# Optimization experiments

Measured on AMD Instinct MI355X. Metric: run time of the kernel, lower is better.

The kernel has to match this reference:

```python
import jax, jax.numpy as jnp
import numpy as np

N_NODES = 100000


def setup_inputs() -> dict:
    key = jax.random.key(0)
    k1, k2, k3, k4 = jax.random.split(key, 4)
    N, E, D = N_NODES, 1200000, 64
    graph_embedding = jax.random.normal(k1, (N, D), dtype=jnp.float32)
    e_feat = jax.random.normal(k2, (E,), dtype=jnp.float32)
    src_idx = jax.random.randint(k3, (E,), 0, N, dtype=jnp.int32)
    dst_idx = jax.random.randint(k4, (E,), 0, N, dtype=jnp.int32)
    return {"graph_embedding": graph_embedding, "e_feat": e_feat,
            "src_idx": src_idx, "dst_idx": dst_idx}


def reference(graph_embedding, e_feat, src_idx, dst_idx):
    # message per edge: concat(src node feature [E,D], edge feature [E,1]) -> [E,D+1]
    e = e_feat.reshape(-1, 1).astype(jnp.float32)          # [E,1]
    msg = jnp.concatenate([graph_embedding[src_idx], e], axis=1)  # [E,D+1]
    # scatter-sum messages to destination nodes -> [N,D+1]
    res = jax.ops.segment_sum(msg, dst_idx, num_segments=N_NODES)
    return res
```

## Files before the change

kernel.cpp:

```cpp
#include <hip/hip_runtime.h>
#include <hip/hip_fp16.h>


#define NB_SHIFT 6
#define BNODES   64
#define SRC_BITS 17
#define SRC_MASK ((1 << SRC_BITS) - 1)
#define BIN_S    4096
#define BIN_T    512
#define MAXNB    2048

__global__ __launch_bounds__(BIN_T) void convhist_kernel(const float* __restrict__ g,
                                                         __half* __restrict__ h,
                                                         int n_emb, int c_blocks,
                                                         const int* __restrict__ dst,
                                                         int* __restrict__ counts,
                                                         int E, int NB) {
    __shared__ int cnt[MAXNB];
    int t = threadIdx.x;

    if (blockIdx.x < c_blocks) {
        int i = (blockIdx.x * BIN_T + t) * 8;
        if (i + 7 < n_emb) {
            float4 a = *(const float4*)(g + i);
            float4 b = *(const float4*)(g + i + 4);
            __half2 h0 = __floats2half2_rn(a.x, a.y);
            __half2 h1 = __floats2half2_rn(a.z, a.w);
            __half2 h2 = __floats2half2_rn(b.x, b.y);
            __half2 h3 = __floats2half2_rn(b.z, b.w);
            int4 o;
            o.x = *(int*)&h0; o.y = *(int*)&h1; o.z = *(int*)&h2; o.w = *(int*)&h3;
            *(int4*)(h + i) = o;
        } else {
            for (int k = i; k < n_emb; ++k) h[k] = __float2half(g[k]);
        }
        return;
    }

    int hb = blockIdx.x - c_blocks;
    for (int i = t; i < MAXNB; i += BIN_T) cnt[i] = 0;
    __syncthreads();
    int e0 = hb * BIN_S + t * 8;
    if (e0 + 7 < E) {
        int4 a = *(const int4*)(dst + e0);
        int4 b = *(const int4*)(dst + e0 + 4);
        atomicAdd(&cnt[a.x >> NB_SHIFT], 1);
        atomicAdd(&cnt[a.y >> NB_SHIFT], 1);
        atomicAdd(&cnt[a.z >> NB_SHIFT], 1);
        atomicAdd(&cnt[a.w >> NB_SHIFT], 1);
        atomicAdd(&cnt[b.x >> NB_SHIFT], 1);
        atomicAdd(&cnt[b.y >> NB_SHIFT], 1);
        atomicAdd(&cnt[b.z >> NB_SHIFT], 1);
        atomicAdd(&cnt[b.w >> NB_SHIFT], 1);
    } else {
        for (int k = e0; k < E; ++k) atomicAdd(&cnt[dst[k] >> NB_SHIFT], 1);
    }
    __syncthreads();
    for (int i = t; i < NB; i += BIN_T)
        if (cnt[i]) atomicAdd(&counts[i], cnt[i]);
}

__global__ void scan_kernel(const int* __restrict__ counts,
                            int* __restrict__ goff, int* __restrict__ gcur,
                            int NB) {
    __shared__ int sh[1024];
    int t = threadIdx.x;
    int c0 = (2 * t     < NB) ? counts[2 * t]     : 0;
    int c1 = (2 * t + 1 < NB) ? counts[2 * t + 1] : 0;
    int s  = c0 + c1;
    sh[t] = s;
    __syncthreads();
    for (int o = 1; o < 1024; o <<= 1) {
        int u = (t >= o) ? sh[t - o] : 0;
        __syncthreads();
        sh[t] += u;
        __syncthreads();
    }
    int ex = sh[t] - s;
    if (2 * t < NB)     { goff[2 * t]     = ex;      gcur[2 * t]     = ex;      }
    if (2 * t + 1 < NB) { goff[2 * t + 1] = ex + c0; gcur[2 * t + 1] = ex + c0; }
    if (t == 1023) goff[NB] = sh[1023];
}

__global__ __launch_bounds__(BIN_T) void bin_kernel(const int* __restrict__ src,
                                                    const float* __restrict__ ef,
                                                    const int* __restrict__ dst,
                                                    int* __restrict__ gcur,
                                                    int2* __restrict__ gpay, int E) {
    __shared__ int cnt[MAXNB];
    __shared__ int lbase[MAXNB];
    __shared__ int wsum[8];
    __shared__ int wbase[8];
    __shared__ int2 stage[BIN_S];
    __shared__ unsigned short sbuck[BIN_S];

    const int t    = threadIdx.x;
    const int lane = t & 63;
    const int wv   = t >> 6;

    for (int i = t; i < MAXNB; i += BIN_T) cnt[i] = 0;
    __syncthreads();

    int e0 = blockIdx.x * BIN_S + t * 8;
    int dv[8], sv[8], bk[8], rk[8];
    float ev[8];

    if (e0 + 7 < E) {
        *(int4*)&dv[0]   = *(const int4*)(dst + e0);
        *(int4*)&dv[4]   = *(const int4*)(dst + e0 + 4);
        *(int4*)&sv[0]   = *(const int4*)(src + e0);
        *(int4*)&sv[4]   = *(const int4*)(src + e0 + 4);
        *(float4*)&ev[0] = *(const float4*)(ef + e0);
        *(float4*)&ev[4] = *(const float4*)(ef + e0 + 4);
#pragma unroll
        for (int k = 0; k < 8; ++k) {
            bk[k] = dv[k] >> NB_SHIFT;
            rk[k] = atomicAdd(&cnt[bk[k]], 1);
        }
    } else {
#pragma unroll
        for (int k = 0; k < 8; ++k) {
            if (e0 + k < E) {
                dv[k] = dst[e0 + k];
                sv[k] = src[e0 + k];
                ev[k] = ef[e0 + k];
                bk[k] = dv[k] >> NB_SHIFT;
                rk[k] = atomicAdd(&cnt[bk[k]], 1);
            } else {
                bk[k] = -1;
            }
        }
    }
    __syncthreads();

    int c0 = cnt[4 * t], c1 = cnt[4 * t + 1], c2 = cnt[4 * t + 2], c3 = cnt[4 * t + 3];
    int ts = c0 + c1 + c2 + c3;
    int incl = ts;
#pragma unroll
    for (int o = 1; o < 64; o <<= 1) {
        int u = __shfl_up(incl, o);
        if (lane >= o) incl += u;
    }
    if (lane == 63) wsum[wv] = incl;
    __syncthreads();
    if (t < 8) {
        int v = wsum[t];
        int inc = v;
#pragma unroll
        for (int o = 1; o < 8; o <<= 1) {
            int u = __shfl_up(inc, o);
            if (t >= o) inc += u;
        }
        wbase[t] = inc - v;
    }
    __syncthreads();
    int ex = wbase[wv] + (incl - ts);
    lbase[4 * t]     = ex;
    lbase[4 * t + 1] = ex + c0;
    lbase[4 * t + 2] = ex + c0 + c1;
    lbase[4 * t + 3] = ex + c0 + c1 + c2;
    __syncthreads();

#pragma unroll
    for (int k = 0; k < 8; ++k) {
        if (bk[k] >= 0) {
            int pos = lbase[bk[k]] + rk[k];
            stage[pos] = make_int2(((dv[k] & (BNODES - 1)) << SRC_BITS) | sv[k],
                                   __float_as_int(ev[k]));
            sbuck[pos] = (unsigned short)bk[k];
        }
    }
    for (int i = t; i < MAXNB; i += BIN_T) {
        int c = cnt[i];
        cnt[i] = (c ? atomicAdd(&gcur[i], c) : 0) - lbase[i];
    }
    __syncthreads();

    int s_total = min(BIN_S, E - blockIdx.x * BIN_S);
    for (int i = t; i < s_total; i += BIN_T) {
        int b = sbuck[i];
        gpay[cnt[b] + i] = stage[i];
    }
}

__global__ __launch_bounds__(256) void bsort_kernel(const int2* __restrict__ gpay,
                                                    const int* __restrict__ goff,
                                                    int* __restrict__ gsrc2,
                                                    int* __restrict__ noff,
                                                    float* __restrict__ out,
                                                    int N, int E) {
    __shared__ int   cnt[BNODES];
    __shared__ int   cur[BNODES];
    __shared__ float esum[BNODES];

    const int t  = threadIdx.x;
    const int b  = blockIdx.x;
    const int lo = goff[b];
    const int hi = goff[b + 1];

    if (t < BNODES) { cnt[t] = 0; esum[t] = 0.f; }
    __syncthreads();

    for (int i = lo + t; i < hi; i += 256)
        atomicAdd(&cnt[gpay[i].x >> SRC_BITS], 1);
    __syncthreads();

    if (t < 64) {
        int v = cnt[t];
        int inc = v;
#pragma unroll
        for (int o = 1; o < 64; o <<= 1) {
            int u = __shfl_up(inc, o);
            if (t >= o) inc += u;
        }
        int base = lo + inc - v;
        cur[t] = base;
        int node = b * BNODES + t;
        if (node <= N) noff[node] = base;
    }
    if (b == 0 && t == 0) noff[N] = E;
    __syncthreads();

    for (int i = lo + t; i < hi; i += 256) {
        int2 p = gpay[i];
        int  r = p.x >> SRC_BITS;
        int pos = atomicAdd(&cur[r], 1);
        gsrc2[pos] = p.x & SRC_MASK;
        atomicAdd(&esum[r], __int_as_float(p.y));
    }
    __syncthreads();

    if (t < 64) {
        int node = b * BNODES + t;
        if (node < N) out[(size_t)node * 65 + 64] = esum[t];
    }
}

__global__ void gather_h_kernel(const __half* __restrict__ hg,
                                const int* __restrict__ gs,
                                const int* __restrict__ noff,
                                float* __restrict__ out, int N) {
    int wid  = (blockIdx.x * blockDim.x + threadIdx.x) >> 6;
    int lane = threadIdx.x & 63;
    if (wid >= N) return;

    int beg = noff[wid];
    int end = noff[wid + 1];

    float a0 = 0.f, a1 = 0.f, a2 = 0.f, a3 = 0.f;
    float a4 = 0.f, a5 = 0.f, a6 = 0.f, a7 = 0.f;
    int j = beg;
    for (; j + 7 < end; j += 8) {
        int s0 = gs[j];     int s1 = gs[j + 1];
        int s2 = gs[j + 2]; int s3 = gs[j + 3];
        int s4 = gs[j + 4]; int s5 = gs[j + 5];
        int s6 = gs[j + 6]; int s7 = gs[j + 7];
        a0 += __half2float(hg[(size_t)s0 * 64 + lane]);
        a1 += __half2float(hg[(size_t)s1 * 64 + lane]);
        a2 += __half2float(hg[(size_t)s2 * 64 + lane]);
        a3 += __half2float(hg[(size_t)s3 * 64 + lane]);
        a4 += __half2float(hg[(size_t)s4 * 64 + lane]);
        a5 += __half2float(hg[(size_t)s5 * 64 + lane]);
        a6 += __half2float(hg[(size_t)s6 * 64 + lane]);
        a7 += __half2float(hg[(size_t)s7 * 64 + lane]);
    }
    for (; j + 3 < end; j += 4) {
        int s0 = gs[j];     int s1 = gs[j + 1];
        int s2 = gs[j + 2]; int s3 = gs[j + 3];
        a0 += __half2float(hg[(size_t)s0 * 64 + lane]);
        a1 += __half2float(hg[(size_t)s1 * 64 + lane]);
        a2 += __half2float(hg[(size_t)s2 * 64 + lane]);
        a3 += __half2float(hg[(size_t)s3 * 64 + lane]);
    }
    for (; j < end; ++j) {
        a0 += __half2float(hg[(size_t)gs[j] * 64 + lane]);
    }
    out[(size_t)wid * 65 + lane] = ((a0 + a1) + (a2 + a3)) + ((a4 + a5) + (a6 + a7));
}


__global__ void atomic_fallback_kernel(const float* __restrict__ gemb,
                                       const float* __restrict__ efeat,
                                       const int* __restrict__ src,
                                       const int* __restrict__ dst,
                                       float* __restrict__ out, int E) {
    int eidx = blockIdx.x * 4 + (threadIdx.x >> 6);
    int lane = threadIdx.x & 63;
    if (eidx >= E) return;
    int s = src[eidx];
    int d = dst[eidx];
    float v = gemb[(size_t)s * 64 + lane];
    atomicAdd(&out[(size_t)d * 65 + lane], v);
    if (lane == 0) atomicAdd(&out[(size_t)d * 65 + 64], efeat[eidx]);
}


extern "C" void kernel_launch(void* const* d_in, const int* in_sizes, int n_in,
                              void* d_out, int out_size, void* d_ws, size_t ws_size,
                              hipStream_t stream) {
    const float* gemb  = (const float*)d_in[0];
    const float* efeat = (const float*)d_in[1];
    const int*   src   = (const int*)d_in[2];
    const int*   dst   = (const int*)d_in[3];
    float*       out   = (float*)d_out;

    const int N  = in_sizes[0] / 64;
    const int E  = in_sizes[1];
    const int NB = (N + BNODES - 1) >> NB_SHIFT;

    auto aln = [](size_t x) { return (x + 15) & ~(size_t)15; };
    size_t off_counts = 0;
    size_t off_goff   = off_counts + aln((size_t)NB * 4);
    size_t off_gcur   = off_goff   + aln((size_t)(NB + 1) * 4);
    size_t off_noff   = off_gcur   + aln((size_t)NB * 4);
    size_t off_gpay   = off_noff   + aln((size_t)(N + 1) * 4);
    size_t off_gsrc2  = off_gpay   + aln((size_t)E * 8);
    size_t off_hg     = off_gsrc2  + aln((size_t)E * 4);
    size_t needed     = off_hg     + (size_t)N * 64 * 2;

    if (N > (1 << SRC_BITS) || NB > MAXNB || ws_size < needed) {
        hipMemsetAsync(d_out, 0, (size_t)out_size * sizeof(float), stream);
        int blocks = (E + 3) / 4;
        atomic_fallback_kernel<<<blocks, 256, 0, stream>>>(gemb, efeat, src, dst, out, E);
        return;
    }

    char*   ws     = (char*)d_ws;
    int*    counts = (int*)(ws + off_counts);
    int*    goff   = (int*)(ws + off_goff);
    int*    gcur   = (int*)(ws + off_gcur);
    int*    noff   = (int*)(ws + off_noff);
    int2*   gpay   = (int2*)(ws + off_gpay);
    int*    gsrc2  = (int*)(ws + off_gsrc2);
    __half* hg     = (__half*)(ws + off_hg);

    hipMemsetAsync(counts, 0, (size_t)NB * 4, stream);

    int n_emb    = N * 64;
    int c_blocks = (n_emb + BIN_T * 8 - 1) / (BIN_T * 8);
    int h_blocks = (E + BIN_S - 1) / BIN_S;
    convhist_kernel<<<c_blocks + h_blocks, BIN_T, 0, stream>>>(
        gemb, hg, n_emb, c_blocks, dst, counts, E, NB);

    scan_kernel<<<1, 1024, 0, stream>>>(counts, goff, gcur, NB);
    bin_kernel<<<h_blocks, BIN_T, 0, stream>>>(src, efeat, dst, gcur, gpay, E);
    bsort_kernel<<<NB, 256, 0, stream>>>(gpay, goff, gsrc2, noff, out, N, E);

    int g_blocks = (N + 3) / 4;
    gather_h_kernel<<<g_blocks, 256, 0, stream>>>(hg, gsrc2, noff, out, N);
}
```

Baseline: 110.1 us.

## Fold bucket scan into bin kernel, split payload arrays, gather half2 per lane

```diff
diff --git a/kernel.cpp b/kernel.cpp
--- a/kernel.cpp
+++ b/kernel.cpp
@@ -60,43 +60,60 @@
         if (cnt[i]) atomicAdd(&counts[i], cnt[i]);
 }
 
-__global__ void scan_kernel(const int* __restrict__ counts,
-                            int* __restrict__ goff, int* __restrict__ gcur,
-                            int NB) {
-    __shared__ int sh[1024];
-    int t = threadIdx.x;
-    int c0 = (2 * t     < NB) ? counts[2 * t]     : 0;
-    int c1 = (2 * t + 1 < NB) ? counts[2 * t + 1] : 0;
-    int s  = c0 + c1;
-    sh[t] = s;
-    __syncthreads();
-    for (int o = 1; o < 1024; o <<= 1) {
-        int u = (t >= o) ? sh[t - o] : 0;
-        __syncthreads();
-        sh[t] += u;
-        __syncthreads();
-    }
-    int ex = sh[t] - s;
-    if (2 * t < NB)     { goff[2 * t]     = ex;      gcur[2 * t]     = ex;      }
-    if (2 * t + 1 < NB) { goff[2 * t + 1] = ex + c0; gcur[2 * t + 1] = ex + c0; }
-    if (t == 1023) goff[NB] = sh[1023];
-}
-
 __global__ __launch_bounds__(BIN_T) void bin_kernel(const int* __restrict__ src,
                                                     const float* __restrict__ ef,
                                                     const int* __restrict__ dst,
-                                                    int* __restrict__ gcur,
-                                                    int2* __restrict__ gpay, int E) {
+                                                    const int* __restrict__ counts,
+                                                    int* __restrict__ gcur0,
+                                                    int* __restrict__ goff,
+                                                    int* __restrict__ gkey,
+                                                    float* __restrict__ gef,
+                                                    int E, int NB) {
     __shared__ int cnt[MAXNB];
     __shared__ int lbase[MAXNB];
     __shared__ int wsum[8];
     __shared__ int wbase[8];
-    __shared__ int2 stage[BIN_S];
+    __shared__ int   skey[BIN_S];
+    __shared__ float sef[BIN_S];
     __shared__ unsigned short sbuck[BIN_S];
 
     const int t    = threadIdx.x;
     const int lane = t & 63;
     const int wv   = t >> 6;
+
+    int4 gc = *(const int4*)(counts + 4 * t);
+    int gts = gc.x + gc.y + gc.z + gc.w;
+    int ginc = gts;
+#pragma unroll
+    for (int o = 1; o < 64; o <<= 1) {
+        int u = __shfl_up(ginc, o);
+        if (lane >= o) ginc += u;
+    }
+    if (lane == 63) wsum[wv] = ginc;
+    __syncthreads();
+    if (t < 8) {
+        int v = wsum[t];
+        int inc = v;
+#pragma unroll
+        for (int o = 1; o < 8; o <<= 1) {
+            int u = __shfl_up(inc, o);
+            if (t >= o) inc += u;
+        }
+        wbase[t] = inc - v;
+    }
+    __syncthreads();
+    int gex = wbase[wv] + (ginc - gts);
+    int sb0 = gex;
+    int sb1 = sb0 + gc.x;
+    int sb2 = sb1 + gc.y;
+    int sb3 = sb2 + gc.z;
+    if (blockIdx.x == 0) {
+        if (4 * t     <= NB) goff[4 * t]     = sb0;
+        if (4 * t + 1 <= NB) goff[4 * t + 1] = sb1;
+        if (4 * t + 2 <= NB) goff[4 * t + 2] = sb2;
+        if (4 * t + 3 <= NB) goff[4 * t + 3] = sb3;
+    }
+    __syncthreads();
 
     for (int i = t; i < MAXNB; i += BIN_T) cnt[i] = 0;
     __syncthreads();
@@ -154,36 +171,46 @@
         wbase[t] = inc - v;
     }
     __syncthreads();
-    int ex = wbase[wv] + (incl - ts);
-    lbase[4 * t]     = ex;
-    lbase[4 * t + 1] = ex + c0;
-    lbase[4 * t + 2] = ex + c0 + c1;
-    lbase[4 * t + 3] = ex + c0 + c1 + c2;
+    int ex  = wbase[wv] + (incl - ts);
+    int lb0 = ex;
+    int lb1 = lb0 + c0;
+    int lb2 = lb1 + c1;
+    int lb3 = lb2 + c2;
+    lbase[4 * t]     = lb0;
+    lbase[4 * t + 1] = lb1;
+    lbase[4 * t + 2] = lb2;
+    lbase[4 * t + 3] = lb3;
     __syncthreads();
 
 #pragma unroll
     for (int k = 0; k < 8; ++k) {
         if (bk[k] >= 0) {
             int pos = lbase[bk[k]] + rk[k];
-            stage[pos] = make_int2(((dv[k] & (BNODES - 1)) << SRC_BITS) | sv[k],
-                                   __float_as_int(ev[k]));
+            skey[pos]  = ((dv[k] & (BNODES - 1)) << SRC_BITS) | sv[k];
+            sef[pos]   = ev[k];
             sbuck[pos] = (unsigned short)bk[k];
         }
     }
-    for (int i = t; i < MAXNB; i += BIN_T) {
-        int c = cnt[i];
-        cnt[i] = (c ? atomicAdd(&gcur[i], c) : 0) - lbase[i];
+    {
+        int f;
+        f = (c0 ? sb0 + atomicAdd(&gcur0[4 * t],     c0) : 0) - lb0; cnt[4 * t]     = f;
+        f = (c1 ? sb1 + atomicAdd(&gcur0[4 * t + 1], c1) : 0) - lb1; cnt[4 * t + 1] = f;
+        f = (c2 ? sb2 + atomicAdd(&gcur0[4 * t + 2], c2) : 0) - lb2; cnt[4 * t + 2] = f;
+        f = (c3 ? sb3 + atomicAdd(&gcur0[4 * t + 3], c3) : 0) - lb3; cnt[4 * t + 3] = f;
     }
     __syncthreads();
 
     int s_total = min(BIN_S, E - blockIdx.x * BIN_S);
     for (int i = t; i < s_total; i += BIN_T) {
         int b = sbuck[i];
-        gpay[cnt[b] + i] = stage[i];
-    }
-}
-
-__global__ __launch_bounds__(256) void bsort_kernel(const int2* __restrict__ gpay,
+        int p = cnt[b] + i;
+        gkey[p] = skey[i];
+        gef[p]  = sef[i];
+    }
+}
+
+__global__ __launch_bounds__(256) void bsort_kernel(const int* __restrict__ gkey,
+                                                    const float* __restrict__ gef,
                                                     const int* __restrict__ goff,
                                                     int* __restrict__ gsrc2,
                                                     int* __restrict__ noff,
@@ -202,7 +229,7 @@
     __syncthreads();
 
     for (int i = lo + t; i < hi; i += 256)
-        atomicAdd(&cnt[gpay[i].x >> SRC_BITS], 1);
+        atomicAdd(&cnt[gkey[i] >> SRC_BITS], 1);
     __syncthreads();
 
     if (t < 64) {
@@ -222,11 +249,11 @@
     __syncthreads();
 
     for (int i = lo + t; i < hi; i += 256) {
-        int2 p = gpay[i];
-        int  r = p.x >> SRC_BITS;
+        int k = gkey[i];
+        int r = k >> SRC_BITS;
         int pos = atomicAdd(&cur[r], 1);
-        gsrc2[pos] = p.x & SRC_MASK;
-        atomicAdd(&esum[r], __int_as_float(p.y));
+        gsrc2[pos] = k & SRC_MASK;
+        atomicAdd(&esum[r], gef[i]);
     }
     __syncthreads();
 
@@ -236,46 +263,66 @@
     }
 }
 
-__global__ void gather_h_kernel(const __half* __restrict__ hg,
-                                const int* __restrict__ gs,
-                                const int* __restrict__ noff,
-                                float* __restrict__ out, int N) {
+__global__ void gather_h2_kernel(const __half* __restrict__ hg,
+                                 const int* __restrict__ gs,
+                                 const int* __restrict__ noff,
+                                 float* __restrict__ out, int N) {
     int wid  = (blockIdx.x * blockDim.x + threadIdx.x) >> 6;
     int lane = threadIdx.x & 63;
     if (wid >= N) return;
 
+    const unsigned int* __restrict__ hg32 = (const unsigned int*)hg;
+    const int hl  = lane >> 5;
+    const int l32 = lane & 31;
+
     int beg = noff[wid];
     int end = noff[wid + 1];
 
-    float a0 = 0.f, a1 = 0.f, a2 = 0.f, a3 = 0.f;
-    float a4 = 0.f, a5 = 0.f, a6 = 0.f, a7 = 0.f;
+    float ax0 = 0.f, ay0 = 0.f, ax1 = 0.f, ay1 = 0.f;
+    float ax2 = 0.f, ay2 = 0.f, ax3 = 0.f, ay3 = 0.f;
+
     int j = beg;
-    for (; j + 7 < end; j += 8) {
-        int s0 = gs[j];     int s1 = gs[j + 1];
-        int s2 = gs[j + 2]; int s3 = gs[j + 3];
-        int s4 = gs[j + 4]; int s5 = gs[j + 5];
-        int s6 = gs[j + 6]; int s7 = gs[j + 7];
-        a0 += __half2float(hg[(size_t)s0 * 64 + lane]);
-        a1 += __half2float(hg[(size_t)s1 * 64 + lane]);
-        a2 += __half2float(hg[(size_t)s2 * 64 + lane]);
-        a3 += __half2float(hg[(size_t)s3 * 64 + lane]);
-        a4 += __half2float(hg[(size_t)s4 * 64 + lane]);
-        a5 += __half2float(hg[(size_t)s5 * 64 + lane]);
-        a6 += __half2float(hg[(size_t)s6 * 64 + lane]);
-        a7 += __half2float(hg[(size_t)s7 * 64 + lane]);
-    }
-    for (; j + 3 < end; j += 4) {
-        int s0 = gs[j];     int s1 = gs[j + 1];
-        int s2 = gs[j + 2]; int s3 = gs[j + 3];
-        a0 += __half2float(hg[(size_t)s0 * 64 + lane]);
-        a1 += __half2float(hg[(size_t)s1 * 64 + lane]);
-        a2 += __half2float(hg[(size_t)s2 * 64 + lane]);
-        a3 += __half2float(hg[(size_t)s3 * 64 + lane]);
-    }
-    for (; j < end; ++j) {
-        a0 += __half2float(hg[(size_t)gs[j] * 64 + lane]);
-    }
-    out[(size_t)wid * 65 + lane] = ((a0 + a1) + (a2 + a3)) + ((a4 + a5) + (a6 + a7));
+    for (; j + 15 < end; j += 16) {
+        int s0 = gs[j +  0 + hl]; int s1 = gs[j +  2 + hl];
+        int s2 = gs[j +  4 + hl]; int s3 = gs[j +  6 + hl];
+        int s4 = gs[j +  8 + hl]; int s5 = gs[j + 10 + hl];
+        int s6 = gs[j + 12 + hl]; int s7 = gs[j + 14 + hl];
+        unsigned int u0 = hg32[(size_t)s0 * 32 + l32];
+        unsigned int u1 = hg32[(size_t)s1 * 32 + l32];
+        unsigned int u2 = hg32[(size_t)s2 * 32 + l32];
+        unsigned int u3 = hg32[(size_t)s3 * 32 + l32];
+        unsigned int u4 = hg32[(size_t)s4 * 32 + l32];
+        unsigned int u5 = hg32[(size_t)s5 * 32 + l32];
+        unsigned int u6 = hg32[(size_t)s6 * 32 + l32];
+        unsigned int u7 = hg32[(size_t)s7 * 32 + l32];
+        __half2 h0 = *(__half2*)&u0; ax0 += __half2float(h0.x); ay0 += __half2float(h0.y);
+        __half2 h1 = *(__half2*)&u1; ax1 += __half2float(h1.x); ay1 += __half2float(h1.y);
+        __half2 h2 = *(__half2*)&u2; ax2 += __half2float(h2.x); ay2 += __half2float(h2.y);
+        __half2 h3 = *(__half2*)&u3; ax3 += __half2float(h3.x); ay3 += __half2float(h3.y);
+        __half2 h4 = *(__half2*)&u4; ax0 += __half2float(h4.x); ay0 += __half2float(h4.y);
+        __half2 h5 = *(__half2*)&u5; ax1 += __half2float(h5.x); ay1 += __half2float(h5.y);
+        __half2 h6 = *(__half2*)&u6; ax2 += __half2float(h6.x); ay2 += __half2float(h6.y);
+        __half2 h7 = *(__half2*)&u7; ax3 += __half2float(h7.x); ay3 += __half2float(h7.y);
+    }
+    for (; j < end; j += 2) {
+        int e = j + hl;
+        unsigned int u = 0;
+        if (e < end) u = hg32[(size_t)gs[e] * 32 + l32];
+        __half2 h = *(__half2*)&u;
+        ax0 += __half2float(h.x);
+        ay0 += __half2float(h.y);
+    }
+
+    float ax = (ax0 + ax1) + (ax2 + ax3);
+    float ay = (ay0 + ay1) + (ay2 + ay3);
+    ax += __shfl_xor(ax, 32);
+    ay += __shfl_xor(ay, 32);
+
+    if (lane < 32) {
+        size_t base = (size_t)wid * 65 + 2 * l32;
+        out[base]     = ax;
+        out[base + 1] = ay;
+    }
 }
 
 
@@ -308,15 +355,16 @@
     const int E  = in_sizes[1];
     const int NB = (N + BNODES - 1) >> NB_SHIFT;
 
-    auto aln = [](size_t x) { return (x + 15) & ~(size_t)15; };
+    auto aln = [](size_t x) { return (x + 63) & ~(size_t)63; };
     size_t off_counts = 0;
-    size_t off_goff   = off_counts + aln((size_t)NB * 4);
-    size_t off_gcur   = off_goff   + aln((size_t)(NB + 1) * 4);
-    size_t off_noff   = off_gcur   + aln((size_t)NB * 4);
-    size_t off_gpay   = off_noff   + aln((size_t)(N + 1) * 4);
-    size_t off_gsrc2  = off_gpay   + aln((size_t)E * 8);
-    size_t off_hg     = off_gsrc2  + aln((size_t)E * 4);
-    size_t needed     = off_hg     + (size_t)N * 64 * 2;
+    size_t off_gcur   = off_counts + (size_t)MAXNB * 4;
+    size_t off_goff   = off_gcur   + (size_t)MAXNB * 4;
+    size_t off_noff   = aln(off_goff + (size_t)(NB + 1) * 4);
+    size_t off_gkey   = aln(off_noff + (size_t)(N + 1) * 4);
+    size_t off_gef    = aln(off_gkey + (size_t)E * 4);
+    size_t off_gsrc2  = aln(off_gef  + (size_t)E * 4);
+    size_t off_hg     = aln(off_gsrc2 + (size_t)E * 4);
+    size_t needed     = off_hg + (size_t)N * 64 * 2;
 
     if (N > (1 << SRC_BITS) || NB > MAXNB || ws_size < needed) {
         hipMemsetAsync(d_out, 0, (size_t)out_size * sizeof(float), stream);
@@ -327,14 +375,15 @@
 
     char*   ws     = (char*)d_ws;
     int*    counts = (int*)(ws + off_counts);
+    int*    gcur0  = (int*)(ws + off_gcur);
     int*    goff   = (int*)(ws + off_goff);
-    int*    gcur   = (int*)(ws + off_gcur);
     int*    noff   = (int*)(ws + off_noff);
-    int2*   gpay   = (int2*)(ws + off_gpay);
+    int*    gkey   = (int*)(ws + off_gkey);
+    float*  gef    = (float*)(ws + off_gef);
     int*    gsrc2  = (int*)(ws + off_gsrc2);
     __half* hg     = (__half*)(ws + off_hg);
 
-    hipMemsetAsync(counts, 0, (size_t)NB * 4, stream);
+    hipMemsetAsync(counts, 0, (size_t)MAXNB * 2 * 4, stream);
 
     int n_emb    = N * 64;
     int c_blocks = (n_emb + BIN_T * 8 - 1) / (BIN_T * 8);
@@ -342,10 +391,10 @@
     convhist_kernel<<<c_blocks + h_blocks, BIN_T, 0, stream>>>(
         gemb, hg, n_emb, c_blocks, dst, counts, E, NB);
 
-    scan_kernel<<<1, 1024, 0, stream>>>(counts, goff, gcur, NB);
-    bin_kernel<<<h_blocks, BIN_T, 0, stream>>>(src, efeat, dst, gcur, gpay, E);
-    bsort_kernel<<<NB, 256, 0, stream>>>(gpay, goff, gsrc2, noff, out, N, E);
+    bin_kernel<<<h_blocks, BIN_T, 0, stream>>>(src, efeat, dst, counts,
+                                               gcur0, goff, gkey, gef, E, NB);
+    bsort_kernel<<<NB, 256, 0, stream>>>(gkey, gef, goff, gsrc2, noff, out, N, E);
 
     int g_blocks = (N + 3) / 4;
-    gather_h_kernel<<<g_blocks, 256, 0, stream>>>(hg, gsrc2, noff, out, N);
-}
+    gather_h2_kernel<<<g_blocks, 256, 0, stream>>>(hg, gsrc2, noff, out, N);
+}
```

Result: slower. 136.3 us (+23.8%).

## Fuse per-bucket sort and gather into one kernel using shared-memory sort

Applied to the files above, without the earlier changes.

```diff
diff --git a/kernel.cpp b/kernel.cpp
--- a/kernel.cpp
+++ b/kernel.cpp
@@ -8,6 +8,8 @@
 #define SRC_MASK ((1 << SRC_BITS) - 1)
 #define BIN_S    4096
 #define BIN_T    512
+#define GAT_T    512
+#define SGCAP    2048
 #define MAXNB    2048
 
 __global__ __launch_bounds__(BIN_T) void convhist_kernel(const float* __restrict__ g,
@@ -183,99 +185,130 @@
     }
 }
 
-__global__ __launch_bounds__(256) void bsort_kernel(const int2* __restrict__ gpay,
-                                                    const int* __restrict__ goff,
-                                                    int* __restrict__ gsrc2,
-                                                    int* __restrict__ noff,
-                                                    float* __restrict__ out,
-                                                    int N, int E) {
+__global__ __launch_bounds__(GAT_T) void bgather_kernel(const __half* __restrict__ hg,
+                                                        const int2* __restrict__ gpay,
+                                                        const int* __restrict__ goff,
+                                                        float* __restrict__ out,
+                                                        int N) {
     __shared__ int   cnt[BNODES];
-    __shared__ int   cur[BNODES];
+    __shared__ int   lb[BNODES];
     __shared__ float esum[BNODES];
-
-    const int t  = threadIdx.x;
-    const int b  = blockIdx.x;
-    const int lo = goff[b];
-    const int hi = goff[b + 1];
-
-    if (t < BNODES) { cnt[t] = 0; esum[t] = 0.f; }
-    __syncthreads();
-
-    for (int i = lo + t; i < hi; i += 256)
-        atomicAdd(&cnt[gpay[i].x >> SRC_BITS], 1);
-    __syncthreads();
-
-    if (t < 64) {
-        int v = cnt[t];
-        int inc = v;
-#pragma unroll
-        for (int o = 1; o < 64; o <<= 1) {
-            int u = __shfl_up(inc, o);
-            if (t >= o) inc += u;
-        }
-        int base = lo + inc - v;
-        cur[t] = base;
-        int node = b * BNODES + t;
-        if (node <= N) noff[node] = base;
-    }
-    if (b == 0 && t == 0) noff[N] = E;
-    __syncthreads();
-
-    for (int i = lo + t; i < hi; i += 256) {
-        int2 p = gpay[i];
-        int  r = p.x >> SRC_BITS;
-        int pos = atomicAdd(&cur[r], 1);
-        gsrc2[pos] = p.x & SRC_MASK;
-        atomicAdd(&esum[r], __int_as_float(p.y));
-    }
-    __syncthreads();
-
-    if (t < 64) {
+    __shared__ int   skey[SGCAP];
+    __shared__ float tile[BNODES * 64];
+
+    const int t    = threadIdx.x;
+    const int b    = blockIdx.x;
+    const int wave = t >> 6;
+    const int lane = t & 63;
+    const int lo   = goff[b];
+    const int hi   = goff[b + 1];
+    const bool multi = (hi - lo) > SGCAP;
+
+    if (t < BNODES) esum[t] = 0.f;
+    if (multi)
+        for (int i = t; i < BNODES * 64; i += GAT_T) tile[i] = 0.f;
+
+    for (int cbase = lo; cbase < hi; cbase += SGCAP) {
+        const int csize = min(SGCAP, hi - cbase);
+
+        __syncthreads();
+        if (t < BNODES) cnt[t] = 0;
+        __syncthreads();
+
+        int kv[4]; int rk[4]; int dr[4];
+#pragma unroll
+        for (int k = 0; k < 4; ++k) {
+            int idx = t + k * GAT_T;
+            dr[k] = -1;
+            if (idx < csize) {
+                int2 p = gpay[cbase + idx];
+                kv[k] = p.x;
+                dr[k] = p.x >> SRC_BITS;
+                rk[k] = atomicAdd(&cnt[dr[k]], 1);
+                atomicAdd(&esum[dr[k]], __int_as_float(p.y));
+            }
+        }
+        __syncthreads();
+
+        if (t < 64) {
+            int v = cnt[t];
+            int inc = v;
+#pragma unroll
+            for (int o = 1; o < 64; o <<= 1) {
+                int u = __shfl_up(inc, o);
+                if (t >= o) inc += u;
+            }
+            lb[t] = inc - v;
+        }
+        __syncthreads();
+
+#pragma unroll
+        for (int k = 0; k < 4; ++k)
+            if (dr[k] >= 0) skey[lb[dr[k]] + rk[k]] = kv[k];
+        __syncthreads();
+
+#pragma unroll
+        for (int i = 0; i < 8; ++i) {
+            const int r  = i * 8 + wave;
+            const int s0 = lb[r];
+            const int c  = cnt[r];
+            float a0 = 0.f, a1 = 0.f, a2 = 0.f, a3 = 0.f;
+            float a4 = 0.f, a5 = 0.f, a6 = 0.f, a7 = 0.f;
+            int j = 0;
+            for (; j + 7 < c; j += 8) {
+                int s_0 = skey[s0 + j]     & SRC_MASK;
+                int s_1 = skey[s0 + j + 1] & SRC_MASK;
+                int s_2 = skey[s0 + j + 2] & SRC_MASK;
+                int s_3 = skey[s0 + j + 3] & SRC_MASK;
+                int s_4 = skey[s0 + j + 4] & SRC_MASK;
+                int s_5 = skey[s0 + j + 5] & SRC_MASK;
+                int s_6 = skey[s0 + j + 6] & SRC_MASK;
+                int s_7 = skey[s0 + j + 7] & SRC_MASK;
+                a0 += __half2float(hg[(size_t)s_0 * 64 + lane]);
+                a1 += __half2float(hg[(size_t)s_1 * 64 + lane]);
+                a2 += __half2float(hg[(size_t)s_2 * 64 + lane]);
+                a3 += __half2float(hg[(size_t)s_3 * 64 + lane]);
+                a4 += __half2float(hg[(size_t)s_4 * 64 + lane]);
+                a5 += __half2float(hg[(size_t)s_5 * 64 + lane]);
+                a6 += __half2float(hg[(size_t)s_6 * 64 + lane]);
+                a7 += __half2float(hg[(size_t)s_7 * 64 + lane]);
+            }
+            for (; j + 3 < c; j += 4) {
+                int s_0 = skey[s0 + j]     & SRC_MASK;
+                int s_1 = skey[s0 + j + 1] & SRC_MASK;
+                int s_2 = skey[s0 + j + 2] & SRC_MASK;
+                int s_3 = skey[s0 + j + 3] & SRC_MASK;
+                a0 += __half2float(hg[(size_t)s_0 * 64 + lane]);
+                a1 += __half2float(hg[(size_t)s_1 * 64 + lane]);
+                a2 += __half2float(hg[(size_t)s_2 * 64 + lane]);
+                a3 += __half2float(hg[(size_t)s_3 * 64 + lane]);
+            }
+            for (; j < c; ++j) {
+                a0 += __half2float(hg[(size_t)(skey[s0 + j] & SRC_MASK) * 64 + lane]);
+            }
+            float sum = ((a0 + a1) + (a2 + a3)) + ((a4 + a5) + (a6 + a7));
+            if (!multi) {
+                int node = b * BNODES + r;
+                if (node < N) out[(size_t)node * 65 + lane] = sum;
+            } else {
+                tile[r * 64 + lane] += sum;
+            }
+        }
+    }
+
+    __syncthreads();
+    if (multi) {
+#pragma unroll
+        for (int i = 0; i < 8; ++i) {
+            int r = i * 8 + wave;
+            int node = b * BNODES + r;
+            if (node < N) out[(size_t)node * 65 + lane] = tile[r * 64 + lane];
+        }
+    }
+    if (t < BNODES) {
         int node = b * BNODES + t;
         if (node < N) out[(size_t)node * 65 + 64] = esum[t];
     }
-}
-
-__global__ void gather_h_kernel(const __half* __restrict__ hg,
-                                const int* __restrict__ gs,
-                                const int* __restrict__ noff,
-                                float* __restrict__ out, int N) {
-    int wid  = (blockIdx.x * blockDim.x + threadIdx.x) >> 6;
-    int lane = threadIdx.x & 63;
-    if (wid >= N) return;
-
-    int beg = noff[wid];
-    int end = noff[wid + 1];
-
-    float a0 = 0.f, a1 = 0.f, a2 = 0.f, a3 = 0.f;
-    float a4 = 0.f, a5 = 0.f, a6 = 0.f, a7 = 0.f;
-    int j = beg;
-    for (; j + 7 < end; j += 8) {
-        int s0 = gs[j];     int s1 = gs[j + 1];
-        int s2 = gs[j + 2]; int s3 = gs[j + 3];
-        int s4 = gs[j + 4]; int s5 = gs[j + 5];
-        int s6 = gs[j + 6]; int s7 = gs[j + 7];
-        a0 += __half2float(hg[(size_t)s0 * 64 + lane]);
-        a1 += __half2float(hg[(size_t)s1 * 64 + lane]);
-        a2 += __half2float(hg[(size_t)s2 * 64 + lane]);
-        a3 += __half2float(hg[(size_t)s3 * 64 + lane]);
-        a4 += __half2float(hg[(size_t)s4 * 64 + lane]);
-        a5 += __half2float(hg[(size_t)s5 * 64 + lane]);
-        a6 += __half2float(hg[(size_t)s6 * 64 + lane]);
-        a7 += __half2float(hg[(size_t)s7 * 64 + lane]);
-    }
-    for (; j + 3 < end; j += 4) {
-        int s0 = gs[j];     int s1 = gs[j + 1];
-        int s2 = gs[j + 2]; int s3 = gs[j + 3];
-        a0 += __half2float(hg[(size_t)s0 * 64 + lane]);
-        a1 += __half2float(hg[(size_t)s1 * 64 + lane]);
-        a2 += __half2float(hg[(size_t)s2 * 64 + lane]);
-        a3 += __half2float(hg[(size_t)s3 * 64 + lane]);
-    }
-    for (; j < end; ++j) {
-        a0 += __half2float(hg[(size_t)gs[j] * 64 + lane]);
-    }
-    out[(size_t)wid * 65 + lane] = ((a0 + a1) + (a2 + a3)) + ((a4 + a5) + (a6 + a7));
 }
 
 
@@ -308,15 +341,13 @@
     const int E  = in_sizes[1];
     const int NB = (N + BNODES - 1) >> NB_SHIFT;
 
-    auto aln = [](size_t x) { return (x + 15) & ~(size_t)15; };
+    auto aln = [](size_t x) { return (x + 63) & ~(size_t)63; };
     size_t off_counts = 0;
-    size_t off_goff   = off_counts + aln((size_t)NB * 4);
-    size_t off_gcur   = off_goff   + aln((size_t)(NB + 1) * 4);
-    size_t off_noff   = off_gcur   + aln((size_t)NB * 4);
-    size_t off_gpay   = off_noff   + aln((size_t)(N + 1) * 4);
-    size_t off_gsrc2  = off_gpay   + aln((size_t)E * 8);
-    size_t off_hg     = off_gsrc2  + aln((size_t)E * 4);
-    size_t needed     = off_hg     + (size_t)N * 64 * 2;
+    size_t off_goff   = off_counts + (size_t)MAXNB * 4;
+    size_t off_gcur   = aln(off_goff + (size_t)(NB + 1) * 4);
+    size_t off_gpay   = aln(off_gcur + (size_t)NB * 4);
+    size_t off_hg     = aln(off_gpay + (size_t)E * 8);
+    size_t needed     = off_hg + (size_t)N * 64 * 2;
 
     if (N > (1 << SRC_BITS) || NB > MAXNB || ws_size < needed) {
         hipMemsetAsync(d_out, 0, (size_t)out_size * sizeof(float), stream);
@@ -329,12 +360,10 @@
     int*    counts = (int*)(ws + off_counts);
     int*    goff   = (int*)(ws + off_goff);
     int*    gcur   = (int*)(ws + off_gcur);
-    int*    noff   = (int*)(ws + off_noff);
     int2*   gpay   = (int2*)(ws + off_gpay);
-    int*    gsrc2  = (int*)(ws + off_gsrc2);
     __half* hg     = (__half*)(ws + off_hg);
 
-    hipMemsetAsync(counts, 0, (size_t)NB * 4, stream);
+    hipMemsetAsync(counts, 0, (size_t)MAXNB * 4, stream);
 
     int n_emb    = N * 64;
     int c_blocks = (n_emb + BIN_T * 8 - 1) / (BIN_T * 8);
@@ -344,8 +373,5 @@
 
     scan_kernel<<<1, 1024, 0, stream>>>(counts, goff, gcur, NB);
     bin_kernel<<<h_blocks, BIN_T, 0, stream>>>(src, efeat, dst, gcur, gpay, E);
-    bsort_kernel<<<NB, 256, 0, stream>>>(gpay, goff, gsrc2, noff, out, N, E);
-
-    int g_blocks = (N + 3) / 4;
-    gather_h_kernel<<<g_blocks, 256, 0, stream>>>(hg, gsrc2, noff, out, N);
-}
+    bgather_kernel<<<NB, GAT_T, 0, stream>>>(hg, gpay, goff, out, N);
+}
```

New measurement: 154.0 us. +39.9%, slower.

## Widen node buckets, compute edge-feature sums via global atomics, shrink payload

Applied to the files above, without the earlier changes.

```diff
diff --git a/kernel.cpp b/kernel.cpp
--- a/kernel.cpp
+++ b/kernel.cpp
@@ -2,19 +2,21 @@
 #include <hip/hip_fp16.h>
 
 
-#define NB_SHIFT 6
-#define BNODES   64
+#define NB_SHIFT 8
+#define BNODES   256
 #define SRC_BITS 17
 #define SRC_MASK ((1 << SRC_BITS) - 1)
 #define BIN_S    4096
 #define BIN_T    512
-#define MAXNB    2048
+#define MAXNB    512
 
 __global__ __launch_bounds__(BIN_T) void convhist_kernel(const float* __restrict__ g,
                                                          __half* __restrict__ h,
                                                          int n_emb, int c_blocks,
                                                          const int* __restrict__ dst,
+                                                         const float* __restrict__ ef,
                                                          int* __restrict__ counts,
+                                                         float* __restrict__ earr,
                                                          int E, int NB) {
     __shared__ int cnt[MAXNB];
     int t = threadIdx.x;
@@ -38,80 +40,98 @@
     }
 
     int hb = blockIdx.x - c_blocks;
-    for (int i = t; i < MAXNB; i += BIN_T) cnt[i] = 0;
+    if (t < MAXNB) cnt[t] = 0;
     __syncthreads();
     int e0 = hb * BIN_S + t * 8;
     if (e0 + 7 < E) {
         int4 a = *(const int4*)(dst + e0);
         int4 b = *(const int4*)(dst + e0 + 4);
-        atomicAdd(&cnt[a.x >> NB_SHIFT], 1);
-        atomicAdd(&cnt[a.y >> NB_SHIFT], 1);
-        atomicAdd(&cnt[a.z >> NB_SHIFT], 1);
-        atomicAdd(&cnt[a.w >> NB_SHIFT], 1);
-        atomicAdd(&cnt[b.x >> NB_SHIFT], 1);
-        atomicAdd(&cnt[b.y >> NB_SHIFT], 1);
-        atomicAdd(&cnt[b.z >> NB_SHIFT], 1);
-        atomicAdd(&cnt[b.w >> NB_SHIFT], 1);
+        float4 fa = *(const float4*)(ef + e0);
+        float4 fb = *(const float4*)(ef + e0 + 4);
+        atomicAdd(&cnt[a.x >> NB_SHIFT], 1);  atomicAdd(&earr[a.x], fa.x);
+        atomicAdd(&cnt[a.y >> NB_SHIFT], 1);  atomicAdd(&earr[a.y], fa.y);
+        atomicAdd(&cnt[a.z >> NB_SHIFT], 1);  atomicAdd(&earr[a.z], fa.z);
+        atomicAdd(&cnt[a.w >> NB_SHIFT], 1);  atomicAdd(&earr[a.w], fa.w);
+        atomicAdd(&cnt[b.x >> NB_SHIFT], 1);  atomicAdd(&earr[b.x], fb.x);
+        atomicAdd(&cnt[b.y >> NB_SHIFT], 1);  atomicAdd(&earr[b.y], fb.y);
+        atomicAdd(&cnt[b.z >> NB_SHIFT], 1);  atomicAdd(&earr[b.z], fb.z);
+        atomicAdd(&cnt[b.w >> NB_SHIFT], 1);  atomicAdd(&earr[b.w], fb.w);
     } else {
-        for (int k = e0; k < E; ++k) atomicAdd(&cnt[dst[k] >> NB_SHIFT], 1);
-    }
-    __syncthreads();
-    for (int i = t; i < NB; i += BIN_T)
-        if (cnt[i]) atomicAdd(&counts[i], cnt[i]);
-}
-
-__global__ void scan_kernel(const int* __restrict__ counts,
-                            int* __restrict__ goff, int* __restrict__ gcur,
-                            int NB) {
-    __shared__ int sh[1024];
-    int t = threadIdx.x;
-    int c0 = (2 * t     < NB) ? counts[2 * t]     : 0;
-    int c1 = (2 * t + 1 < NB) ? counts[2 * t + 1] : 0;
-    int s  = c0 + c1;
-    sh[t] = s;
-    __syncthreads();
-    for (int o = 1; o < 1024; o <<= 1) {
-        int u = (t >= o) ? sh[t - o] : 0;
-        __syncthreads();
-        sh[t] += u;
-        __syncthreads();
-    }
-    int ex = sh[t] - s;
-    if (2 * t < NB)     { goff[2 * t]     = ex;      gcur[2 * t]     = ex;      }
-    if (2 * t + 1 < NB) { goff[2 * t + 1] = ex + c0; gcur[2 * t + 1] = ex + c0; }
-    if (t == 1023) goff[NB] = sh[1023];
+        for (int k = e0; k < E; ++k) {
+            int d = dst[k];
+            atomicAdd(&cnt[d >> NB_SHIFT], 1);
+            atomicAdd(&earr[d], ef[k]);
+        }
+    }
+    __syncthreads();
+    if (t < NB && cnt[t]) atomicAdd(&counts[t], cnt[t]);
+}
+
+__global__ __launch_bounds__(512) void scan_kernel(const int* __restrict__ counts,
+                                                   int* __restrict__ goff,
+                                                   int* __restrict__ gcur,
+                                                   int* __restrict__ noff,
+                                                   int NB, int N) {
+    __shared__ int wsum[8];
+    __shared__ int wbase[8];
+    int t    = threadIdx.x;
+    int lane = t & 63;
+    int wv   = t >> 6;
+    int v    = (t < NB) ? counts[t] : 0;
+    int incl = v;
+#pragma unroll
+    for (int o = 1; o < 64; o <<= 1) {
+        int u = __shfl_up(incl, o);
+        if (lane >= o) incl += u;
+    }
+    if (lane == 63) wsum[wv] = incl;
+    __syncthreads();
+    if (t < 8) {
+        int s = wsum[t];
+        int inc = s;
+#pragma unroll
+        for (int o = 1; o < 8; o <<= 1) {
+            int u = __shfl_up(inc, o);
+            if (t >= o) inc += u;
+        }
+        wbase[t] = inc - s;
+    }
+    __syncthreads();
+    int ex = wbase[wv] + (incl - v);
+    if (t < NB) { goff[t] = ex; gcur[t] = ex; }
+    if (t == 511) {
+        int total = wbase[7] + incl;
+        goff[NB] = total;
+        noff[N]  = total;
+    }
 }
 
 __global__ __launch_bounds__(BIN_T) void bin_kernel(const int* __restrict__ src,
-                                                    const float* __restrict__ ef,
                                                     const int* __restrict__ dst,
                                                     int* __restrict__ gcur,
-                                                    int2* __restrict__ gpay, int E) {
+                                                    int* __restrict__ gkey, int E) {
     __shared__ int cnt[MAXNB];
     __shared__ int lbase[MAXNB];
     __shared__ int wsum[8];
     __shared__ int wbase[8];
-    __shared__ int2 stage[BIN_S];
+    __shared__ int skey[BIN_S];
     __shared__ unsigned short sbuck[BIN_S];
 
     const int t    = threadIdx.x;
     const int lane = t & 63;
     const int wv   = t >> 6;
 
-    for (int i = t; i < MAXNB; i += BIN_T) cnt[i] = 0;
+    cnt[t] = 0;
     __syncthreads();
 
     int e0 = blockIdx.x * BIN_S + t * 8;
     int dv[8], sv[8], bk[8], rk[8];
-    float ev[8];
 
     if (e0 + 7 < E) {
-        *(int4*)&dv[0]   = *(const int4*)(dst + e0);
-        *(int4*)&dv[4]   = *(const int4*)(dst + e0 + 4);
-        *(int4*)&sv[0]   = *(const int4*)(src + e0);
-        *(int4*)&sv[4]   = *(const int4*)(src + e0 + 4);
-        *(float4*)&ev[0] = *(const float4*)(ef + e0);
-        *(float4*)&ev[4] = *(const float4*)(ef + e0 + 4);
+        *(int4*)&dv[0] = *(const int4*)(dst + e0);
+        *(int4*)&dv[4] = *(const int4*)(dst + e0 + 4);
+        *(int4*)&sv[0] = *(const int4*)(src + e0);
+        *(int4*)&sv[4] = *(const int4*)(src + e0 + 4);
 #pragma unroll
         for (int k = 0; k < 8; ++k) {
             bk[k] = dv[k] >> NB_SHIFT;
@@ -123,7 +143,6 @@
             if (e0 + k < E) {
                 dv[k] = dst[e0 + k];
                 sv[k] = src[e0 + k];
-                ev[k] = ef[e0 + k];
                 bk[k] = dv[k] >> NB_SHIFT;
                 rk[k] = atomicAdd(&cnt[bk[k]], 1);
             } else {
@@ -133,9 +152,8 @@
     }
     __syncthreads();
 
-    int c0 = cnt[4 * t], c1 = cnt[4 * t + 1], c2 = cnt[4 * t + 2], c3 = cnt[4 * t + 3];
-    int ts = c0 + c1 + c2 + c3;
-    int incl = ts;
+    int c = cnt[t];
+    int incl = c;
 #pragma unroll
     for (int o = 1; o < 64; o <<= 1) {
         int u = __shfl_up(incl, o);
@@ -144,101 +162,94 @@
     if (lane == 63) wsum[wv] = incl;
     __syncthreads();
     if (t < 8) {
-        int v = wsum[t];
-        int inc = v;
+        int s = wsum[t];
+        int inc = s;
 #pragma unroll
         for (int o = 1; o < 8; o <<= 1) {
             int u = __shfl_up(inc, o);
             if (t >= o) inc += u;
         }
-        wbase[t] = inc - v;
-    }
-    __syncthreads();
-    int ex = wbase[wv] + (incl - ts);
-    lbase[4 * t]     = ex;
-    lbase[4 * t + 1] = ex + c0;
-    lbase[4 * t + 2] = ex + c0 + c1;
-    lbase[4 * t + 3] = ex + c0 + c1 + c2;
+        wbase[t] = inc - s;
+    }
+    __syncthreads();
+    int lb = wbase[wv] + (incl - c);
+    lbase[t] = lb;
     __syncthreads();
 
 #pragma unroll
     for (int k = 0; k < 8; ++k) {
         if (bk[k] >= 0) {
             int pos = lbase[bk[k]] + rk[k];
-            stage[pos] = make_int2(((dv[k] & (BNODES - 1)) << SRC_BITS) | sv[k],
-                                   __float_as_int(ev[k]));
+            skey[pos]  = ((dv[k] & (BNODES - 1)) << SRC_BITS) | sv[k];
             sbuck[pos] = (unsigned short)bk[k];
         }
     }
-    for (int i = t; i < MAXNB; i += BIN_T) {
-        int c = cnt[i];
-        cnt[i] = (c ? atomicAdd(&gcur[i], c) : 0) - lbase[i];
-    }
+    cnt[t] = (c ? atomicAdd(&gcur[t], c) : 0) - lb;
     __syncthreads();
 
     int s_total = min(BIN_S, E - blockIdx.x * BIN_S);
     for (int i = t; i < s_total; i += BIN_T) {
-        int b = sbuck[i];
-        gpay[cnt[b] + i] = stage[i];
-    }
-}
-
-__global__ __launch_bounds__(256) void bsort_kernel(const int2* __restrict__ gpay,
+        gkey[cnt[sbuck[i]] + i] = skey[i];
+    }
+}
+
+__global__ __launch_bounds__(512) void bsort_kernel(const int* __restrict__ gkey,
                                                     const int* __restrict__ goff,
                                                     int* __restrict__ gsrc2,
                                                     int* __restrict__ noff,
-                                                    float* __restrict__ out,
-                                                    int N, int E) {
-    __shared__ int   cnt[BNODES];
-    __shared__ int   cur[BNODES];
-    __shared__ float esum[BNODES];
+                                                    int N) {
+    __shared__ int cnt[BNODES];
+    __shared__ int cur[BNODES];
 
     const int t  = threadIdx.x;
     const int b  = blockIdx.x;
     const int lo = goff[b];
     const int hi = goff[b + 1];
 
-    if (t < BNODES) { cnt[t] = 0; esum[t] = 0.f; }
-    __syncthreads();
-
-    for (int i = lo + t; i < hi; i += 256)
-        atomicAdd(&cnt[gpay[i].x >> SRC_BITS], 1);
+    if (t < BNODES) cnt[t] = 0;
+    __syncthreads();
+
+    for (int i = lo + t; i < hi; i += 512)
+        atomicAdd(&cnt[gkey[i] >> SRC_BITS], 1);
     __syncthreads();
 
     if (t < 64) {
-        int v = cnt[t];
-        int inc = v;
+        int c0 = cnt[4 * t], c1 = cnt[4 * t + 1], c2 = cnt[4 * t + 2], c3 = cnt[4 * t + 3];
+        int ts = c0 + c1 + c2 + c3;
+        int inc = ts;
 #pragma unroll
         for (int o = 1; o < 64; o <<= 1) {
             int u = __shfl_up(inc, o);
             if (t >= o) inc += u;
         }
-        int base = lo + inc - v;
-        cur[t] = base;
-        int node = b * BNODES + t;
-        if (node <= N) noff[node] = base;
-    }
-    if (b == 0 && t == 0) noff[N] = E;
-    __syncthreads();
-
-    for (int i = lo + t; i < hi; i += 256) {
-        int2 p = gpay[i];
-        int  r = p.x >> SRC_BITS;
-        int pos = atomicAdd(&cur[r], 1);
-        gsrc2[pos] = p.x & SRC_MASK;
-        atomicAdd(&esum[r], __int_as_float(p.y));
-    }
-    __syncthreads();
-
-    if (t < 64) {
-        int node = b * BNODES + t;
-        if (node < N) out[(size_t)node * 65 + 64] = esum[t];
+        int ex = inc - ts;
+        int b0 = lo + ex;
+        int b1 = b0 + c0;
+        int b2 = b1 + c1;
+        int b3 = b2 + c2;
+        cur[4 * t]     = b0;
+        cur[4 * t + 1] = b1;
+        cur[4 * t + 2] = b2;
+        cur[4 * t + 3] = b3;
+        int node = b * BNODES + 4 * t;
+        if (node     < N) noff[node]     = b0;
+        if (node + 1 < N) noff[node + 1] = b1;
+        if (node + 2 < N) noff[node + 2] = b2;
+        if (node + 3 < N) noff[node + 3] = b3;
+    }
+    __syncthreads();
+
+    for (int i = lo + t; i < hi; i += 512) {
+        int k = gkey[i];
+        int pos = atomicAdd(&cur[k >> SRC_BITS], 1);
+        gsrc2[pos] = k & SRC_MASK;
     }
 }
 
 __global__ void gather_h_kernel(const __half* __restrict__ hg,
                                 const int* __restrict__ gs,
                                 const int* __restrict__ noff,
+                                const float* __restrict__ earr,
                                 float* __restrict__ out, int N) {
     int wid  = (blockIdx.x * blockDim.x + threadIdx.x) >> 6;
     int lane = threadIdx.x & 63;
@@ -276,6 +287,7 @@
         a0 += __half2float(hg[(size_t)gs[j] * 64 + lane]);
     }
     out[(size_t)wid * 65 + lane] = ((a0 + a1) + (a2 + a3)) + ((a4 + a5) + (a6 + a7));
+    if (lane == 0) out[(size_t)wid * 65 + 64] = earr[wid];
 }
 
 
@@ -308,15 +320,16 @@
     const int E  = in_sizes[1];
     const int NB = (N + BNODES - 1) >> NB_SHIFT;
 
-    auto aln = [](size_t x) { return (x + 15) & ~(size_t)15; };
+    auto aln = [](size_t x) { return (x + 63) & ~(size_t)63; };
     size_t off_counts = 0;
-    size_t off_goff   = off_counts + aln((size_t)NB * 4);
-    size_t off_gcur   = off_goff   + aln((size_t)(NB + 1) * 4);
-    size_t off_noff   = off_gcur   + aln((size_t)NB * 4);
-    size_t off_gpay   = off_noff   + aln((size_t)(N + 1) * 4);
-    size_t off_gsrc2  = off_gpay   + aln((size_t)E * 8);
-    size_t off_hg     = off_gsrc2  + aln((size_t)E * 4);
-    size_t needed     = off_hg     + (size_t)N * 64 * 2;
+    size_t off_earr   = off_counts + (size_t)MAXNB * 4;
+    size_t off_goff   = aln(off_earr + (size_t)N * 4);
+    size_t off_gcur   = aln(off_goff + (size_t)(NB + 1) * 4);
+    size_t off_noff   = aln(off_gcur + (size_t)NB * 4);
+    size_t off_gkey   = aln(off_noff + (size_t)(N + 1) * 4);
+    size_t off_gsrc2  = aln(off_gkey + (size_t)E * 4);
+    size_t off_hg     = aln(off_gsrc2 + (size_t)E * 4);
+    size_t needed     = off_hg + (size_t)N * 64 * 2;
 
     if (N > (1 << SRC_BITS) || NB > MAXNB || ws_size < needed) {
         hipMemsetAsync(d_out, 0, (size_t)out_size * sizeof(float), stream);
@@ -327,25 +340,26 @@
 
     char*   ws     = (char*)d_ws;
     int*    counts = (int*)(ws + off_counts);
+    float*  earr   = (float*)(ws + off_earr);
     int*    goff   = (int*)(ws + off_goff);
     int*    gcur   = (int*)(ws + off_gcur);
     int*    noff   = (int*)(ws + off_noff);
-    int2*   gpay   = (int2*)(ws + off_gpay);
+    int*    gkey   = (int*)(ws + off_gkey);
     int*    gsrc2  = (int*)(ws + off_gsrc2);
     __half* hg     = (__half*)(ws + off_hg);
 
-    hipMemsetAsync(counts, 0, (size_t)NB * 4, stream);
+    hipMemsetAsync(counts, 0, (size_t)MAXNB * 4 + (size_t)N * 4, stream);
 
     int n_emb    = N * 64;
     int c_blocks = (n_emb + BIN_T * 8 - 1) / (BIN_T * 8);
     int h_blocks = (E + BIN_S - 1) / BIN_S;
     convhist_kernel<<<c_blocks + h_blocks, BIN_T, 0, stream>>>(
-        gemb, hg, n_emb, c_blocks, dst, counts, E, NB);
-
-    scan_kernel<<<1, 1024, 0, stream>>>(counts, goff, gcur, NB);
-    bin_kernel<<<h_blocks, BIN_T, 0, stream>>>(src, efeat, dst, gcur, gpay, E);
-    bsort_kernel<<<NB, 256, 0, stream>>>(gpay, goff, gsrc2, noff, out, N, E);
+        gemb, hg, n_emb, c_blocks, dst, efeat, counts, earr, E, NB);
+
+    scan_kernel<<<1, 512, 0, stream>>>(counts, goff, gcur, noff, NB, N);
+    bin_kernel<<<h_blocks, BIN_T, 0, stream>>>(src, dst, gcur, gkey, E);
+    bsort_kernel<<<NB, 512, 0, stream>>>(gkey, goff, gsrc2, noff, N);
 
     int g_blocks = (N + 3) / 4;
-    gather_h_kernel<<<g_blocks, 256, 0, stream>>>(hg, gsrc2, noff, out, N);
-}
+    gather_h_kernel<<<g_blocks, 256, 0, stream>>>(hg, gsrc2, noff, earr, out, N);
+}
```

New measurement: 164.3 us. +49.2%, slower.
